# Performance work log

Hardware: AMD Instinct MI355X
Metric: run time of the kernel (lower is better)

## Reference

```python
import jax, jax.numpy as jnp
from jax import lax
import numpy as np

A = 9                 # 3 scales x 3 ratios
PRE_NMS_TOPN = 4000
POST_NMS_TOPN = 2000
NMS_THRESH = 0.7
MIN_SIZE = 16.0       # min_size * im_scale (im_info scale = 1)
NEG_INF = -1e9


def generate_anchors(base_size=16, ratios=(0.5, 1.0, 2.0), scales=(8, 16, 32)):
    ratios = np.array(ratios, dtype=np.float64)
    scales = np.array(scales, dtype=np.float64)
    w = h = float(base_size)
    xc = yc = 0.5 * (base_size - 1)
    size = w * h
    ws_r = np.round(np.sqrt(size / ratios))          # [3]
    hs_r = np.round(ws_r * ratios)                   # [3]
    ws = (ws_r[:, None] * scales[None, :]).reshape(-1)   # [9]
    hs = (hs_r[:, None] * scales[None, :]).reshape(-1)   # [9]
    anchors = np.stack([xc - 0.5 * (ws - 1), yc - 0.5 * (hs - 1),
                        xc + 0.5 * (ws - 1), yc + 0.5 * (hs - 1)], axis=1)
    return anchors.astype(np.float32)                # [9,4]


def _conv(x, w, b, padding):
    y = lax.conv_general_dilated(x, w, (1, 1), padding,
                                 dimension_numbers=('NCHW', 'OIHW', 'NCHW'))
    return y + b[None, :, None, None]


def _bbox_transform_inv(anchors, deltas):
    w = anchors[:, 2] - anchors[:, 0] + 1.0
    h = anchors[:, 3] - anchors[:, 1] + 1.0
    cx = anchors[:, 0] + 0.5 * w
    cy = anchors[:, 1] + 0.5 * h
    pcx = deltas[:, 0] * w + cx
    pcy = deltas[:, 1] * h + cy
    pw = jnp.exp(deltas[:, 2]) * w
    ph = jnp.exp(deltas[:, 3]) * h
    return jnp.stack([pcx - 0.5 * pw, pcy - 0.5 * ph,
                      pcx + 0.5 * pw, pcy + 0.5 * ph], axis=1)


def _greedy_nms(boxes, keep_init, thresh):
    # boxes already sorted by descending score; keep_init masks invalid rows
    x1, y1, x2, y2 = boxes[:, 0], boxes[:, 1], boxes[:, 2], boxes[:, 3]
    areas = (x2 - x1 + 1.0) * (y2 - y1 + 1.0)
    xx1 = jnp.maximum(x1[:, None], x1[None, :])
    yy1 = jnp.maximum(y1[:, None], y1[None, :])
    xx2 = jnp.minimum(x2[:, None], x2[None, :])
    yy2 = jnp.minimum(y2[:, None], y2[None, :])
    inter = jnp.maximum(0.0, xx2 - xx1 + 1.0) * jnp.maximum(0.0, yy2 - yy1 + 1.0)
    iou = inter / (areas[:, None] + areas[None, :] - inter)   # [N,N]
    n = boxes.shape[0]
    idx = jnp.arange(n)

    def body(i, keep):
        suppress = keep[i] & (iou[i] > thresh) & (idx > i)
        return keep & ~suppress

    return lax.fori_loop(0, n, body, keep_init)


def reference(im, feats, w_conv, b_conv, w_cls, b_cls, w_reg, b_reg):
    im_h, im_w = im.shape[2], im.shape[3]
    fh, fw = feats.shape[2], feats.shape[3]
    stride = round(im_w / fw)

    # RPN head (classifier)
    hid = jax.nn.relu(_conv(feats, w_conv, b_conv, 'SAME'))
    rpn_map = _conv(hid, w_cls, b_cls, 'SAME')       # [1, 2A, fh, fw]
    rpn_bbox = _conv(hid, w_reg, b_reg, 'SAME')      # [1, 4A, fh, fw]

    # anchor generation: [K*A, 4], shift-major / anchor-minor
    base = jnp.asarray(generate_anchors())
    sx = jnp.arange(fw, dtype=jnp.float32) * stride
    sy = jnp.arange(fh, dtype=jnp.float32) * stride
    sxx, syy = jnp.meshgrid(sx, sy)                  # [fh, fw]
    shifts = jnp.stack([sxx.ravel(), syy.ravel(), sxx.ravel(), syy.ravel()], 1)
    anchors = (base[None, :, :] + shifts[:, None, :]).reshape(-1, 4)

    # predictions, flattened in (h, w, a) order to match anchors
    deltas = rpn_bbox.transpose(0, 2, 3, 1).reshape(-1, 4)
    scores = rpn_map[:, A:, :, :].transpose(0, 2, 3, 1).reshape(-1)

    proposals = _bbox_transform_inv(anchors, deltas)
    # clip_boxes to image
    proposals = jnp.stack([
        jnp.clip(proposals[:, 0], 0.0, im_w - 1.0),
        jnp.clip(proposals[:, 1], 0.0, im_h - 1.0),
        jnp.clip(proposals[:, 2], 0.0, im_w - 1.0),
        jnp.clip(proposals[:, 3], 0.0, im_h - 1.0)], axis=1)

    # filter_boxes (min_size) expressed as a score mask (jit-friendly)
    ws = proposals[:, 2] - proposals[:, 0] + 1.0
    hs = proposals[:, 3] - proposals[:, 1] + 1.0
    valid = (ws >= MIN_SIZE) & (hs >= MIN_SIZE)
    masked_scores = jnp.where(valid, scores, NEG_INF)

    # sort descending, take pre_nms_topN
    order = jnp.argsort(-masked_scores)[:PRE_NMS_TOPN]
    top_boxes = proposals[order]
    top_scores = masked_scores[order]
    keep_init = top_scores > NEG_INF / 2

    keep = _greedy_nms(top_boxes, keep_init, NMS_THRESH)

    # take first post_nms_topN kept (already in score order), padded with zeros
    rank = jnp.cumsum(keep) - 1
    take = keep & (rank < POST_NMS_TOPN)
    dst = jnp.where(take, rank, 0)
    out_boxes = jnp.zeros((POST_NMS_TOPN, 4), dtype=top_boxes.dtype)
    out_boxes = out_boxes.at[dst].add(jnp.where(take[:, None], top_boxes, 0.0))
    out_scores = jnp.zeros((POST_NMS_TOPN, 1), dtype=top_scores.dtype)
    out_scores = out_scores.at[dst].add(jnp.where(take[:, None], top_scores[:, None], 0.0))
    return out_boxes, out_scores


def setup_inputs() -> dict:
    key = jax.random.key(0)
    ks = jax.random.split(key, 8)
    # small weight scale keeps exp(dw) in a sane range, as a trained RPN would
    return {
        'im': jax.random.normal(ks[0], (1, 3, 800, 1216), jnp.float32),
        'feats': jax.random.normal(ks[1], (1, 1024, 50, 76), jnp.float32),
        'w_conv': jax.random.normal(ks[2], (512, 1024, 3, 3), jnp.float32) * 0.001,
        'b_conv': jnp.zeros((512,), jnp.float32),
        'w_cls': jax.random.normal(ks[3], (18, 512, 1, 1), jnp.float32) * 0.01,
        'b_cls': jnp.zeros((18,), jnp.float32),
        'w_reg': jax.random.normal(ks[4], (36, 512, 1, 1), jnp.float32) * 0.01,
        'b_reg': jnp.zeros((36,), jnp.float32),
    }
```

## Files before the change

### kernel.cpp

```cpp
#include <hip/hip_runtime.h>
#include <stdint.h>
#include <math.h>

typedef unsigned long long u64;
typedef unsigned int u32;

#define CIN     1024
#define COUT    512
#define FH      50
#define FW      76
#define QP      80
#define HIDP    4096
#define FPITCH  4160
#define NPOS    3800
#define NA      34200
#define PRE_N   4000
#define POST_N  2000
#define MASKW   63
#define TBN     4032
#define KSLICES 8
#define CPS     128
#define QT      128

#define P0 (3*CIN*FPITCH)
#define P2 (512*48)
#define P3 65536

__device__ __forceinline__ void async16(const float* g, float* l) {
  __builtin_amdgcn_global_load_lds(
      (__attribute__((address_space(1))) void*)(g),
      (__attribute__((address_space(3))) void*)(l), 16, 0, 0);
}

__global__ void k_prep(const float* __restrict__ feats,
                       const float* __restrict__ w_cls, const float* __restrict__ b_cls,
                       const float* __restrict__ w_reg, const float* __restrict__ b_reg,
                       float* __restrict__ fpad3, float* __restrict__ wT, float* __restrict__ bT,
                       u32* __restrict__ hist, u32* __restrict__ ctrl,
                       double4* __restrict__ tb, float* __restrict__ ts) {
  int idx = blockIdx.x * 256 + threadIdx.x;
  if (idx < P0) {
    int tc = idx / (CIN * FPITCH);
    int rem = idx - tc * (CIN * FPITCH);
    int cin = rem / FPITCH;
    int j = rem - cin * FPITCH + tc;
    float v = 0.f;
    if (j < FPITCH) {
      int r = j / QP, u = j - r * QP;
      if (r >= 1 && r <= FH && u >= 1 && u <= FW)
        v = feats[cin * (FH * FW) + (r - 1) * FW + (u - 1)];
    }
    fpad3[idx] = v;
    return;
  }
  idx -= P0;
  if (idx < P2) {
    int c = idx / 48, o = idx - c * 48;
    float v = 0.f;
    if (o < 9) v = w_cls[(size_t)(9 + o) * 512 + c];
    else if (o < 45) v = w_reg[(size_t)(o - 9) * 512 + c];
    wT[idx] = v;
    return;
  }
  idx -= P2;
  if (idx < P3) {
    hist[idx] = 0;
    if (idx < 8) ctrl[idx] = 0;
    if (idx < 48) bT[idx] = (idx < 9) ? b_cls[9 + idx] : (idx < 45 ? b_reg[idx - 9] : 0.f);
    if (idx >= PRE_N && idx < TBN) { tb[idx] = make_double4(0.0, 0.0, 0.0, 0.0); ts[idx] = -1.0e9f; }
  }
}

__global__ void k_wt(const float* __restrict__ w, float* __restrict__ wt) {
  __shared__ float t[64][65];
  int k0 = blockIdx.x * 64, oc0 = blockIdx.y * 64;
  int tx = threadIdx.x & 63, tg = threadIdx.x >> 6;
#pragma unroll
  for (int rr = 0; rr < 16; rr++) {
    int row = tg * 16 + rr;
    t[row][tx] = w[(size_t)(oc0 + row) * 9216 + k0 + tx];
  }
  __syncthreads();
#pragma unroll
  for (int rr = 0; rr < 16; rr++) {
    int kr = tg * 16 + rr;
    wt[(size_t)(k0 + kr) * 512 + oc0 + tx] = t[tx][kr];
  }
}

__global__ __launch_bounds__(256, 6) void k_conv(const float* __restrict__ fpad3,
                                                 const float* __restrict__ wt,
                                                 float* __restrict__ hidp) {
  __shared__ __align__(16) float Bl[3][10][QT];
  const int tid = threadIdx.x;
  const int lane = tid & 63;
  const int wv = __builtin_amdgcn_readfirstlane(tid >> 6);
  const int q0 = blockIdx.x * QT;
  const int ws = (blockIdx.y << 2) + wv;
  const int c0 = blockIdx.z * CPS;

  int rA = 2 * wv + (lane >> 5);
  int trA = rA / 3, tcA = rA - trA * 3;
  u32 voffA = (u32)tcA * (CIN * FPITCH) + (u32)trA * QP + q0 + (lane & 31) * 4;
  u32 voffB = 2u * (CIN * FPITCH) + 2u * QP + q0 + (lane & 31) * 4;

  float acc32[8][2];
  double acc64[8][2];
#pragma unroll
  for (int i = 0; i < 8; i++) {
    acc32[i][0] = acc32[i][1] = 0.f;
    acc64[i][0] = acc64[i][1] = 0.0;
  }

#define STAGE(buf, s)  do {                                                     \
    const float* _b = fpad3 + (size_t)(c0 + (s)) * FPITCH;                      \
    async16(_b + voffA, &Bl[buf][2 * wv][0]);                                   \
    if (wv == 0) async16(_b + voffB, &Bl[buf][8][0]);                           \
  } while (0)

  STAGE(0, 0);
  STAGE(1, 1);

#pragma unroll 1
  for (int s = 0; s < CPS; s++) {
    if (s + 1 < CPS) {
      if (wv == 0) asm volatile("s_waitcnt vmcnt(2)" ::: "memory");
      else         asm volatile("s_waitcnt vmcnt(1)" ::: "memory");
    } else {
      asm volatile("s_waitcnt vmcnt(0)" ::: "memory");
    }
    __builtin_amdgcn_s_barrier();
    __builtin_amdgcn_sched_barrier(0);
    const int b0 = s % 3;
    if (s + 2 < CPS) STAGE((s + 2) % 3, s + 2);
    const float* wp = wt + ((size_t)(c0 + s) * 9 << 9) + (ws << 3);
#pragma unroll
    for (int ks = 0; ks < 9; ks++) {
      float2 b2 = *(const float2*)&Bl[b0][ks][lane * 2];
      const float* w8 = wp + (ks << 9);
#pragma unroll
      for (int i = 0; i < 8; i++) {
        float w = w8[i];
        acc32[i][0] = fmaf(w, b2.x, acc32[i][0]);
        acc32[i][1] = fmaf(w, b2.y, acc32[i][1]);
      }
    }
    if ((s & 7) == 7) {
#pragma unroll
      for (int i = 0; i < 8; i++) {
        acc64[i][0] += (double)acc32[i][0]; acc32[i][0] = 0.f;
        acc64[i][1] += (double)acc32[i][1]; acc32[i][1] = 0.f;
      }
    }
  }
#undef STAGE

#pragma unroll
  for (int i = 0; i < 8; i++) {
    float2 o;
    o.x = (float)acc64[i][0];
    o.y = (float)acc64[i][1];
    *(float2*)&hidp[((size_t)(blockIdx.z * COUT + (ws << 3) + i) << 12) + q0 + lane * 2] = o;
  }
}

__global__ void k_reduce(const float* __restrict__ hidp, const float* __restrict__ bconv,
                         float* __restrict__ hid) {
  int idx = blockIdx.x * 256 + threadIdx.x;
  int oc = idx >> 12;
  double s = 0.0;
#pragma unroll
  for (int z = 0; z < KSLICES; z++)
    s += (double)hidp[idx + ((size_t)z << 21)];
  s += (double)bconv[oc];
  hid[idx] = s > 0.0 ? (float)s : 0.f;
}

__global__ __launch_bounds__(256, 8) void k_head(const float* __restrict__ hid,
                                                 const float* __restrict__ wT,
                                                 const float* __restrict__ bT,
                                                 float* __restrict__ scoresb,
                                                 float* __restrict__ deltab) {
  int lane = threadIdx.x & 63;
  int wv = threadIdx.x >> 6;
  int q = blockIdx.x * 64 + lane;
  int og = blockIdx.y * 12 + wv * 3;
  double acc0 = 0.0, acc1 = 0.0, acc2 = 0.0;
#pragma unroll 4
  for (int c = 0; c < 512; c++) {
    double hv = (double)hid[((size_t)c << 12) + q];
    const float* wr = wT + c * 48 + og;
    acc0 += hv * (double)wr[0];
    acc1 += hv * (double)wr[1];
    acc2 += hv * (double)wr[2];
  }
  int y = q / QP, x = q - y * QP;
  if (x < FW && y < FH) {
    int pos = y * FW + x;
    double a[3] = {acc0, acc1, acc2};
#pragma unroll
    for (int j = 0; j < 3; j++) {
      int o = og + j;
      float r = (float)(a[j] + (double)bT[o]);
      if (o < 9)       scoresb[o * NPOS + pos] = r;
      else if (o < 45) deltab[(o - 9) * NPOS + pos] = r;
    }
  }
}

__device__ __constant__ float AW[9] = {184.f, 368.f, 736.f, 128.f, 256.f, 512.f, 88.f, 176.f, 352.f};
__device__ __constant__ float AH[9] = {96.f, 192.f, 384.f, 128.f, 256.f, 512.f, 176.f, 352.f, 704.f};

__global__ void k_prop(const float* __restrict__ scoresb, const float* __restrict__ deltab,
                       double4* __restrict__ boxesd, u64* __restrict__ keys,
                       float* __restrict__ smask, u32* __restrict__ hist,
                       float* __restrict__ dout) {
  int g = blockIdx.x * 256 + threadIdx.x;
  if (g < 10000) dout[g] = 0.f;
  if (g >= NA) return;
  int pos = g / 9, a = g - pos * 9;
  int y = pos / FW, x = pos - y * FW;
  double w = (double)AW[a], h = (double)AH[a];
  double cx = x * 16.0 + 8.0, cy = y * 16.0 + 8.0;
  double d0 = (double)deltab[(4 * a + 0) * NPOS + pos];
  double d1 = (double)deltab[(4 * a + 1) * NPOS + pos];
  double d2 = (double)deltab[(4 * a + 2) * NPOS + pos];
  double d3 = (double)deltab[(4 * a + 3) * NPOS + pos];
  double pcx = d0 * w + cx, pcy = d1 * h + cy;
  double pw = exp(d2) * w, ph = exp(d3) * h;
  double px1 = fmin(fmax(pcx - 0.5 * pw, 0.0), 1215.0);
  double py1 = fmin(fmax(pcy - 0.5 * ph, 0.0), 799.0);
  double px2 = fmin(fmax(pcx + 0.5 * pw, 0.0), 1215.0);
  double py2 = fmin(fmax(pcy + 0.5 * ph, 0.0), 799.0);
  bool valid = (px2 - px1 + 1.0 >= 16.0) && (py2 - py1 + 1.0 >= 16.0);
  float sc = scoresb[a * NPOS + pos];
  float ms = valid ? sc : -1.0e9f;
  boxesd[g] = make_double4(px1, py1, px2, py2);
  smask[g] = ms;
  u32 u = __float_as_uint(ms);
  u = (u >> 31) ? ~u : (u | 0x80000000u);
  keys[g] = ((u64)u << 32) | (u32)(~(u32)g);
  atomicAdd(&hist[u >> 16], 1u);
}

__global__ void k_scan(const u32* __restrict__ hist, u32* __restrict__ ctrl) {
  __shared__ u32 cs[256];
  __shared__ u32 sfx[256];
  int t = threadIdx.x;
  u32 s = 0;
  for (int i = 0; i < 256; i++) s += hist[t * 256 + i];
  cs[t] = s;
  __syncthreads();
  if (t == 0) {
    u32 c = 0;
    for (int i = 255; i >= 0; i--) { sfx[i] = c; c += cs[i]; }
  }
  __syncthreads();
  u32 before = sfx[t];
  u32 c = 0;
  for (int b = 255; b >= 0; b--) {
    u32 hv = hist[t * 256 + b];
    if (before + c < PRE_N && before + c + hv >= PRE_N) {
      ctrl[0] = (u32)(t * 256 + b);
      ctrl[1] = before + c;
    }
    c += hv;
  }
}

__global__ void k_compact(const u64* __restrict__ keys, u32* __restrict__ ctrl,
                          u64* __restrict__ candK, u32* __restrict__ candG) {
  int g = blockIdx.x * 256 + threadIdx.x;
  if (g >= NA) return;
  u32 binB = ctrl[0];
  u64 k = keys[g];
  if ((u32)(k >> 48) >= binB) {
    u32 idx = atomicAdd(&ctrl[2], 1u);
    candK[idx] = k;
    candG[idx] = g;
  }
}

__global__ void k_rank(const u64* __restrict__ candK, const u32* __restrict__ candG,
                       const u32* __restrict__ ctrl, const double4* __restrict__ boxesd,
                       const float* __restrict__ smask, double4* __restrict__ tb,
                       float* __restrict__ ts) {
  __shared__ u64 kk[256];
  u32 m = ctrl[2];
  if (blockIdx.x * 256 >= m) return;
  int i = blockIdx.x * 256 + threadIdx.x;
  u64 my = (i < (int)m) ? candK[i] : 0ULL;
  u32 rank = 0;
  for (u32 base = 0; base < m; base += 256) {
    u32 j = base + threadIdx.x;
    kk[threadIdx.x] = (j < m) ? candK[j] : 0ULL;
    __syncthreads();
    u32 lim = m - base; if (lim > 256) lim = 256;
    for (u32 tt = 0; tt < lim; tt++) rank += (kk[tt] > my) ? 1u : 0u;
    __syncthreads();
  }
  if (i < (int)m && rank < PRE_N) {
    u32 g = candG[i];
    tb[rank] = boxesd[g];
    ts[rank] = smask[g];
  }
}

__global__ void k_mask(const double4* __restrict__ tb, u64* __restrict__ mask) {
  __shared__ double4 bx[64];
  int w = blockIdx.x;
  int i = blockIdx.y * 256 + threadIdx.x;
  if (threadIdx.x < 64) bx[threadIdx.x] = tb[w * 64 + threadIdx.x];
  __syncthreads();
  if (i >= PRE_N) return;
  double4 b = tb[i];
  double ai = (b.z - b.x + 1.0) * (b.w - b.y + 1.0);
  u64 word = 0;
#pragma unroll 8
  for (int j = 0; j < 64; j++) {
    int jg = w * 64 + j;
    double4 cc = bx[j];
    double xx1 = fmax(b.x, cc.x), yy1 = fmax(b.y, cc.y);
    double xx2 = fmin(b.z, cc.z), yy2 = fmin(b.w, cc.w);
    double iw = xx2 - xx1 + 1.0, ih = yy2 - yy1 + 1.0;
    iw = iw > 0.0 ? iw : 0.0; ih = ih > 0.0 ? ih : 0.0;
    double inter = iw * ih;
    double aj = (cc.z - cc.x + 1.0) * (cc.w - cc.y + 1.0);
    bool sup = (jg > i) && (inter > 0.7 * (ai + aj - inter));
    word |= sup ? (1ULL << j) : 0ULL;
  }
  mask[(size_t)i * MASKW + w] = word;
}

__global__ __launch_bounds__(64, 1) void k_nms(const u64* __restrict__ mask,
                                               const float* __restrict__ ts,
                                               const double4* __restrict__ tb,
                                               float* __restrict__ out) {
  int lane = threadIdx.x;
  u64 keep = 0;
  for (int w = 0; w < MASKW; w++) {
    float s = ts[w * 64 + lane];
    u64 b = __ballot(s > -5.0e8f);
    if (lane == w) keep = b;
  }
  for (int c = 0; c < MASKW; c++) {
    u64 cur = __shfl(keep, c);
    u64 D = mask[(size_t)(c * 64 + lane) * MASKW + c];
    for (int j = 0; j < 64; j++) {
      u64 Dj = __shfl(D, j);
      if ((cur >> j) & 1ULL) cur &= ~Dj;
    }
    if (lane == c) keep = cur;
    u64 supp = 0;
#pragma unroll 1
    for (int jb = 0; jb < 64; jb += 16) {
      u64 v[16];
#pragma unroll
      for (int u2 = 0; u2 < 16; u2++)
        v[u2] = (lane < MASKW && lane >= c) ? mask[(size_t)(c * 64 + jb + u2) * MASKW + lane] : 0ULL;
#pragma unroll
      for (int u2 = 0; u2 < 16; u2++)
        if ((cur >> (jb + u2)) & 1ULL) supp |= v[u2];
    }
    keep &= ~supp;
  }
  int pc = __popcll(keep);
  int pre = pc;
#pragma unroll
  for (int off = 1; off < 64; off <<= 1) {
    int v = __shfl_up(pre, off);
    if (lane >= off) pre += v;
  }
  pre -= pc;
#pragma unroll 1
  for (int j = 0; j < 64; j++) {
    if ((keep >> j) & 1ULL) {
      int r = pre + __popcll(keep & ((1ULL << j) - 1ULL));
      if (r < POST_N) {
        int i = lane * 64 + j;
        double4 b = tb[i];
        out[r * 4 + 0] = (float)b.x;
        out[r * 4 + 1] = (float)b.y;
        out[r * 4 + 2] = (float)b.z;
        out[r * 4 + 3] = (float)b.w;
        out[8000 + r] = ts[i];
      }
    }
  }
}

extern "C" void kernel_launch(void* const* d_in, const int* in_sizes, int n_in,
                              void* d_out, int out_size, void* d_ws, size_t ws_size,
                              hipStream_t stream) {
  const float* feats  = (const float*)d_in[1];
  const float* w_conv = (const float*)d_in[2];
  const float* b_conv = (const float*)d_in[3];
  const float* w_cls  = (const float*)d_in[4];
  const float* b_cls  = (const float*)d_in[5];
  const float* w_reg  = (const float*)d_in[6];
  const float* b_reg  = (const float*)d_in[7];
  float* out = (float*)d_out;

  char* p = (char*)d_ws;
  auto carve = [&p](size_t bytes) -> void* {
    void* r = (void*)p;
    p += (bytes + 255) & ~(size_t)255;
    return r;
  };
  float*   fpad3   = (float*)carve(sizeof(float) * (P0 + 512));
  float*   wt      = (float*)carve(sizeof(float) * 9216 * 512);
  float*   wT      = (float*)carve(sizeof(float) * P2);
  float*   bT      = (float*)carve(sizeof(float) * 48);
  float*   hid     = (float*)carve(sizeof(float) * COUT * HIDP);
  float*   hidp    = (float*)carve(sizeof(float) * KSLICES * COUT * HIDP);
  float*   scoresb = (float*)carve(sizeof(float) * 9 * NPOS);
  float*   deltab  = (float*)carve(sizeof(float) * 36 * NPOS);
  double4* boxesd  = (double4*)carve(sizeof(double4) * NA);
  u64*     keys    = (u64*)carve(sizeof(u64) * NA);
  float*   smask   = (float*)carve(sizeof(float) * NA);
  u32*     hist    = (u32*)carve(sizeof(u32) * 65536);
  u32*     ctrl    = (u32*)carve(256);
  u64*     candK   = (u64*)carve(sizeof(u64) * NA);
  u32*     candG   = (u32*)carve(sizeof(u32) * NA);
  double4* tb      = (double4*)carve(sizeof(double4) * TBN);
  float*   ts      = (float*)carve(sizeof(float) * TBN);
  u64*     maskb   = (u64*)carve(sizeof(u64) * (size_t)TBN * MASKW);
  (void)ws_size; (void)in_sizes; (void)n_in; (void)out_size;

  int prep_blocks = (P0 + P2 + P3) / 256;
  k_prep<<<prep_blocks, 256, 0, stream>>>(feats, w_cls, b_cls, w_reg, b_reg,
                                          fpad3, wT, bT, hist, ctrl, tb, ts);
  k_wt<<<dim3(144, 8), 256, 0, stream>>>(w_conv, wt);
  k_conv<<<dim3(32, 16, KSLICES), 256, 0, stream>>>(fpad3, wt, hidp);
  k_reduce<<<8192, 256, 0, stream>>>(hidp, b_conv, hid);
  k_head<<<dim3(64, 4), 256, 0, stream>>>(hid, wT, bT, scoresb, deltab);
  k_prop<<<134, 256, 0, stream>>>(scoresb, deltab, boxesd, keys, smask, hist, out);
  k_scan<<<1, 256, 0, stream>>>(hist, ctrl);
  k_compact<<<134, 256, 0, stream>>>(keys, ctrl, candK, candG);
  k_rank<<<134, 256, 0, stream>>>(candK, candG, ctrl, boxesd, smask, tb, ts);
  k_mask<<<dim3(MASKW, 16), 256, 0, stream>>>(tb, maskb);
  k_nms<<<1, 64, 0, stream>>>(maskb, ts, tb, out);
}
```

Measured before the change: 1.111 ms.

## Fuse weight transpose into prep, double-buffer conv, prefetch NMS mask rows

Merges the weight-transpose kernel into the prep kernel as extra blocks, saving one launch. In the conv kernel, the triple-buffered LDS staging with hand-written vmcnt waits becomes a double buffer with __syncthreads, weights load as float4 with a three-deep register prefetch, and occupancy is lowered to 5. The histogram bin index is transposed so the scan reads it coalesced, and the NMS kernel preloads all 64 mask words per chunk and uses branchless mask updates. The trade-off is higher register pressure in both conv and NMS, and less load latency hidden in conv now that only one stage is in flight.

```diff
diff --git a/kernel.cpp b/kernel.cpp
--- a/kernel.cpp
+++ b/kernel.cpp
@@ -25,6 +25,8 @@
 #define P0 (3*CIN*FPITCH)
 #define P2 (512*48)
 #define P3 65536
+#define PREP_BLKS ((P0+P2+P3)/256)
+#define WT_BLKS   (144*8)
 
 __device__ __forceinline__ void async16(const float* g, float* l) {
   __builtin_amdgcn_global_load_lds(
@@ -32,12 +34,32 @@
       (__attribute__((address_space(3))) void*)(l), 16, 0, 0);
 }
 
-__global__ void k_prep(const float* __restrict__ feats,
+__global__ void k_prep(const float* __restrict__ feats, const float* __restrict__ w_conv,
                        const float* __restrict__ w_cls, const float* __restrict__ b_cls,
                        const float* __restrict__ w_reg, const float* __restrict__ b_reg,
-                       float* __restrict__ fpad3, float* __restrict__ wT, float* __restrict__ bT,
+                       float* __restrict__ fpad3, float* __restrict__ wt,
+                       float* __restrict__ wT, float* __restrict__ bT,
                        u32* __restrict__ hist, u32* __restrict__ ctrl,
                        double4* __restrict__ tb, float* __restrict__ ts) {
+  __shared__ float t[64][65];
+  if (blockIdx.x >= PREP_BLKS) {
+    int bt_ = blockIdx.x - PREP_BLKS;
+    int kx = bt_ % 144, oy = bt_ / 144;
+    int k0 = kx * 64, oc0 = oy * 64;
+    int tx = threadIdx.x & 63, tg = threadIdx.x >> 6;
+#pragma unroll
+    for (int rr = 0; rr < 16; rr++) {
+      int row = tg * 16 + rr;
+      t[row][tx] = w_conv[(size_t)(oc0 + row) * 9216 + k0 + tx];
+    }
+    __syncthreads();
+#pragma unroll
+    for (int rr = 0; rr < 16; rr++) {
+      int kr = tg * 16 + rr;
+      wt[(size_t)(k0 + kr) * 512 + oc0 + tx] = t[tx][kr];
+    }
+    return;
+  }
   int idx = blockIdx.x * 256 + threadIdx.x;
   if (idx < P0) {
     int tc = idx / (CIN * FPITCH);
@@ -71,27 +93,10 @@
   }
 }
 
-__global__ void k_wt(const float* __restrict__ w, float* __restrict__ wt) {
-  __shared__ float t[64][65];
-  int k0 = blockIdx.x * 64, oc0 = blockIdx.y * 64;
-  int tx = threadIdx.x & 63, tg = threadIdx.x >> 6;
-#pragma unroll
-  for (int rr = 0; rr < 16; rr++) {
-    int row = tg * 16 + rr;
-    t[row][tx] = w[(size_t)(oc0 + row) * 9216 + k0 + tx];
-  }
-  __syncthreads();
-#pragma unroll
-  for (int rr = 0; rr < 16; rr++) {
-    int kr = tg * 16 + rr;
-    wt[(size_t)(k0 + kr) * 512 + oc0 + tx] = t[tx][kr];
-  }
-}
-
-__global__ __launch_bounds__(256, 6) void k_conv(const float* __restrict__ fpad3,
+__global__ __launch_bounds__(256, 5) void k_conv(const float* __restrict__ fpad3,
                                                  const float* __restrict__ wt,
                                                  float* __restrict__ hidp) {
-  __shared__ __align__(16) float Bl[3][10][QT];
+  __shared__ __align__(16) float Bl[2][10][QT];
   const int tid = threadIdx.x;
   const int lane = tid & 63;
   const int wv = __builtin_amdgcn_readfirstlane(tid >> 6);
@@ -99,6 +104,9 @@
   const int ws = (blockIdx.y << 2) + wv;
   const int c0 = blockIdx.z * CPS;
 
+  int vzero;
+  asm("v_mov_b32 %0, 0" : "=v"(vzero));
+
   int rA = 2 * wv + (lane >> 5);
   int trA = rA / 3, tcA = rA - trA * 3;
   u32 voffA = (u32)tcA * (CIN * FPITCH) + (u32)trA * QP + q0 + (lane & 31) * 4;
@@ -111,6 +119,8 @@
     acc32[i][0] = acc32[i][1] = 0.f;
     acc64[i][0] = acc64[i][1] = 0.0;
   }
+
+  const float* wbase = wt + (((size_t)c0 * 9) << 9) + (ws << 3) + vzero;
 
 #define STAGE(buf, s)  do {                                                     \
     const float* _b = fpad3 + (size_t)(c0 + (s)) * FPITCH;                      \
@@ -119,31 +129,43 @@
   } while (0)
 
   STAGE(0, 0);
-  STAGE(1, 1);
 
 #pragma unroll 1
   for (int s = 0; s < CPS; s++) {
-    if (s + 1 < CPS) {
-      if (wv == 0) asm volatile("s_waitcnt vmcnt(2)" ::: "memory");
-      else         asm volatile("s_waitcnt vmcnt(1)" ::: "memory");
-    } else {
-      asm volatile("s_waitcnt vmcnt(0)" ::: "memory");
-    }
-    __builtin_amdgcn_s_barrier();
-    __builtin_amdgcn_sched_barrier(0);
-    const int b0 = s % 3;
-    if (s + 2 < CPS) STAGE((s + 2) % 3, s + 2);
-    const float* wp = wt + ((size_t)(c0 + s) * 9 << 9) + (ws << 3);
+    __syncthreads();
+    if (s + 1 < CPS) STAGE((s + 1) & 1, s + 1);
+    const int b0 = s & 1;
+    const float* wstep = wbase + ((size_t)(s * 9) << 9);
+    float4 w0[3], w1[3];
+#pragma unroll
+    for (int k = 0; k < 3; k++) {
+      w0[k] = *(const float4*)(wstep + ((size_t)k << 9));
+      w1[k] = *(const float4*)(wstep + ((size_t)k << 9) + 4);
+    }
 #pragma unroll
     for (int ks = 0; ks < 9; ks++) {
       float2 b2 = *(const float2*)&Bl[b0][ks][lane * 2];
-      const float* w8 = wp + (ks << 9);
-#pragma unroll
-      for (int i = 0; i < 8; i++) {
-        float w = w8[i];
-        acc32[i][0] = fmaf(w, b2.x, acc32[i][0]);
-        acc32[i][1] = fmaf(w, b2.y, acc32[i][1]);
+      float4 wA = w0[ks % 3], wB = w1[ks % 3];
+      if (ks + 3 < 9) {
+        w0[ks % 3] = *(const float4*)(wstep + ((size_t)(ks + 3) << 9));
+        w1[ks % 3] = *(const float4*)(wstep + ((size_t)(ks + 3) << 9) + 4);
       }
+      acc32[0][0] = fmaf(wA.x, b2.x, acc32[0][0]);
+      acc32[0][1] = fmaf(wA.x, b2.y, acc32[0][1]);
+      acc32[1][0] = fmaf(wA.y, b2.x, acc32[1][0]);
+      acc32[1][1] = fmaf(wA.y, b2.y, acc32[1][1]);
+      acc32[2][0] = fmaf(wA.z, b2.x, acc32[2][0]);
+      acc32[2][1] = fmaf(wA.z, b2.y, acc32[2][1]);
+      acc32[3][0] = fmaf(wA.w, b2.x, acc32[3][0]);
+      acc32[3][1] = fmaf(wA.w, b2.y, acc32[3][1]);
+      acc32[4][0] = fmaf(wB.x, b2.x, acc32[4][0]);
+      acc32[4][1] = fmaf(wB.x, b2.y, acc32[4][1]);
+      acc32[5][0] = fmaf(wB.y, b2.x, acc32[5][0]);
+      acc32[5][1] = fmaf(wB.y, b2.y, acc32[5][1]);
+      acc32[6][0] = fmaf(wB.z, b2.x, acc32[6][0]);
+      acc32[6][1] = fmaf(wB.z, b2.y, acc32[6][1]);
+      acc32[7][0] = fmaf(wB.w, b2.x, acc32[7][0]);
+      acc32[7][1] = fmaf(wB.w, b2.y, acc32[7][1]);
     }
     if ((s & 7) == 7) {
 #pragma unroll
@@ -240,7 +262,7 @@
   u32 u = __float_as_uint(ms);
   u = (u >> 31) ? ~u : (u | 0x80000000u);
   keys[g] = ((u64)u << 32) | (u32)(~(u32)g);
-  atomicAdd(&hist[u >> 16], 1u);
+  atomicAdd(&hist[(((u >> 16) & 0xFFu) << 8) | (u >> 24)], 1u);
 }
 
 __global__ void k_scan(const u32* __restrict__ hist, u32* __restrict__ ctrl) {
@@ -248,7 +270,7 @@
   __shared__ u32 sfx[256];
   int t = threadIdx.x;
   u32 s = 0;
-  for (int i = 0; i < 256; i++) s += hist[t * 256 + i];
+  for (int i = 0; i < 256; i++) s += hist[(i << 8) | t];
   cs[t] = s;
   __syncthreads();
   if (t == 0) {
@@ -258,10 +280,10 @@
   __syncthreads();
   u32 before = sfx[t];
   u32 c = 0;
-  for (int b = 255; b >= 0; b--) {
-    u32 hv = hist[t * 256 + b];
+  for (int blo = 255; blo >= 0; blo--) {
+    u32 hv = hist[(blo << 8) | t];
     if (before + c < PRE_N && before + c + hv >= PRE_N) {
-      ctrl[0] = (u32)(t * 256 + b);
+      ctrl[0] = (u32)(t * 256 + blo);
       ctrl[1] = before + c;
     }
     c += hv;
@@ -344,23 +366,25 @@
     if (lane == w) keep = b;
   }
   for (int c = 0; c < MASKW; c++) {
+    u64 D = mask[(size_t)(c * 64 + lane) * MASKW + c];
+    const bool ld = (lane < MASKW) && (lane >= c);
+    u64 v[64];
+#pragma unroll
+    for (int j = 0; j < 64; j++)
+      v[j] = ld ? mask[(size_t)(c * 64 + j) * MASKW + lane] : 0ULL;
     u64 cur = __shfl(keep, c);
-    u64 D = mask[(size_t)(c * 64 + lane) * MASKW + c];
+#pragma unroll 1
     for (int j = 0; j < 64; j++) {
       u64 Dj = __shfl(D, j);
-      if ((cur >> j) & 1ULL) cur &= ~Dj;
+      u64 msk = (u64)0 - ((cur >> j) & 1ULL);
+      cur &= ~(Dj & msk);
     }
     if (lane == c) keep = cur;
     u64 supp = 0;
-#pragma unroll 1
-    for (int jb = 0; jb < 64; jb += 16) {
-      u64 v[16];
-#pragma unroll
-      for (int u2 = 0; u2 < 16; u2++)
-        v[u2] = (lane < MASKW && lane >= c) ? mask[(size_t)(c * 64 + jb + u2) * MASKW + lane] : 0ULL;
-#pragma unroll
-      for (int u2 = 0; u2 < 16; u2++)
-        if ((cur >> (jb + u2)) & 1ULL) supp |= v[u2];
+#pragma unroll
+    for (int j = 0; j < 64; j++) {
+      u64 msk = (u64)0 - ((cur >> j) & 1ULL);
+      supp |= v[j] & msk;
     }
     keep &= ~supp;
   }
@@ -368,8 +392,8 @@
   int pre = pc;
 #pragma unroll
   for (int off = 1; off < 64; off <<= 1) {
-    int v = __shfl_up(pre, off);
-    if (lane >= off) pre += v;
+    int v2 = __shfl_up(pre, off);
+    if (lane >= off) pre += v2;
   }
   pre -= pc;
 #pragma unroll 1
@@ -427,10 +451,8 @@
   u64*     maskb   = (u64*)carve(sizeof(u64) * (size_t)TBN * MASKW);
   (void)ws_size; (void)in_sizes; (void)n_in; (void)out_size;
 
-  int prep_blocks = (P0 + P2 + P3) / 256;
-  k_prep<<<prep_blocks, 256, 0, stream>>>(feats, w_cls, b_cls, w_reg, b_reg,
-                                          fpad3, wT, bT, hist, ctrl, tb, ts);
-  k_wt<<<dim3(144, 8), 256, 0, stream>>>(w_conv, wt);
+  k_prep<<<PREP_BLKS + WT_BLKS, 256, 0, stream>>>(feats, w_conv, w_cls, b_cls, w_reg, b_reg,
+                                                  fpad3, wt, wT, bT, hist, ctrl, tb, ts);
   k_conv<<<dim3(32, 16, KSLICES), 256, 0, stream>>>(fpad3, wt, hidp);
   k_reduce<<<8192, 256, 0, stream>>>(hidp, b_conv, hid);
   k_head<<<dim3(64, 4), 256, 0, stream>>>(hid, wT, bT, scoresb, deltab);
```

After: 1.973 ms. 1.78x slower.
